# Kernel optimization log

Measured on AMD Instinct MI355X. Metric: run time of the kernel, lower is better.

Reference implementation:

```python
import math
import jax, jax.numpy as jnp
import numpy as np

B, T, D, H, HD, FF = 2, 2048, 768, 12, 64, 3072


def setup_inputs() -> dict:
    key = jax.random.key(0)
    ks = jax.random.split(key, 9)
    s = 0.02  # init scale
    x = jax.random.normal(ks[0], (B, T, D), jnp.float32)
    wq = jax.random.normal(ks[1], (D, D), jnp.float32) * s
    wk = jax.random.normal(ks[2], (D, D), jnp.float32) * s
    wv = jax.random.normal(ks[3], (D, D), jnp.float32) * s
    wo = jax.random.normal(ks[4], (D, D), jnp.float32) * s
    w1 = jax.random.normal(ks[5], (FF, D), jnp.float32) * s
    w2 = jax.random.normal(ks[6], (FF, D), jnp.float32) * s
    w3 = jax.random.normal(ks[7], (D, FF), jnp.float32) * s
    attn_norm_w = jnp.ones((D,), jnp.float32)
    ffn_norm_w = jnp.ones((D,), jnp.float32)
    # interleaved RoPE cache: values pair-repeated along head_dim
    inv_freq = 1.0 / (10000.0 ** (np.arange(0, HD, 2, dtype=np.float32) / HD))
    freqs = np.arange(T, dtype=np.float32)[:, None] * inv_freq[None, :]  # [T, HD/2]
    emb = np.repeat(freqs, 2, axis=-1)  # [T, HD]
    cos = jnp.asarray(np.cos(emb), jnp.float32)[None, None]  # [1,1,T,HD]
    sin = jnp.asarray(np.sin(emb), jnp.float32)[None, None]
    return {"x": x, "wq": wq, "wk": wk, "wv": wv, "wo": wo,
            "w1": w1, "w2": w2, "w3": w3,
            "attn_norm_w": attn_norm_w, "ffn_norm_w": ffn_norm_w,
            "cos": cos, "sin": sin}


def _rmsnorm(x, w, eps=1e-6):
    n = jnp.linalg.norm(x, axis=-1, keepdims=True)
    return w * x / (n / math.sqrt(x.shape[-1]) + eps)


def _rotate_half(x):
    x1, x2 = x[..., ::2], x[..., 1::2]
    return jnp.stack((-x2, x1), axis=-1).reshape(x.shape)


def _attention(x, wq, wk, wv, wo, cos, sin):
    b, t, c = x.shape
    q = (x @ wq.T).reshape(b, t, H, HD).transpose(0, 2, 1, 3)  # [B,H,T,hd]
    k = (x @ wk.T).reshape(b, t, H, HD).transpose(0, 2, 1, 3)
    v = (x @ wv.T).reshape(b, t, H, HD).transpose(0, 2, 1, 3)
    c_, s_ = cos[:, :, :t, :], sin[:, :, :t, :]
    q = q * c_ + _rotate_half(q) * s_
    k = k * c_ + _rotate_half(k) * s_
    att = jnp.einsum('bhqd,bhkd->bhqk', q, k) / math.sqrt(HD)
    mask = jnp.triu(jnp.full((t, t), -jnp.inf, att.dtype), k=1)
    att = jax.nn.softmax(att + mask, axis=-1)
    y = jnp.einsum('bhqk,bhkd->bhqd', att, v)
    y = y.transpose(0, 2, 1, 3).reshape(b, t, c)
    return y @ wo.T


def reference(x, wq, wk, wv, wo, w1, w2, w3, attn_norm_w, ffn_norm_w, cos, sin):
    x = x + _attention(_rmsnorm(x, attn_norm_w), wq, wk, wv, wo, cos, sin)
    h = _rmsnorm(x, ffn_norm_w)
    ff = (jax.nn.silu(h @ w1.T) * (h @ w2.T)) @ w3.T
    return x + ff
```

## Files before the change

### kernel.cpp

```cpp
#include <hip/hip_runtime.h>
#include <hip/hip_bf16.h>
#include <math.h>

typedef __bf16 bf16;
typedef __bf16 bf16x4 __attribute__((ext_vector_type(4)));
typedef __bf16 bf16x8 __attribute__((ext_vector_type(8)));
typedef float floatx4 __attribute__((ext_vector_type(4)));

#define T_ 2048
#define D_ 768
#define H_ 12
#define HD_ 64
#define FF_ 3072
#define LOG2E 1.44269504f
#define LDP 72

__device__ __forceinline__ floatx4 mfma_bf16(bf16x8 a, bf16x8 b, floatx4 c) {
  return __builtin_amdgcn_mfma_f32_16x16x32_bf16(a, b, c, 0, 0, 0);
}

__global__ __launch_bounds__(256)
void cvt_k(const float* __restrict__ wq, const float* __restrict__ wk,
           const float* __restrict__ wv, const float* __restrict__ wo,
           const float* __restrict__ w1, const float* __restrict__ w2,
           const float* __restrict__ w3, bf16* __restrict__ o) {
  const long i = ((long)blockIdx.x * 256 + threadIdx.x) * 8;
  const float* s;
  if      (i <  589824) s = wq + i;
  else if (i < 1179648) s = wk + (i -  589824);
  else if (i < 1769472) s = wv + (i - 1179648);
  else if (i < 2359296) s = wo + (i - 1769472);
  else if (i < 4718592) s = w1 + (i - 2359296);
  else if (i < 7077888) s = w2 + (i - 4718592);
  else                  s = w3 + (i - 7077888);
  const floatx4 a = *(const floatx4*)s;
  const floatx4 b = *(const floatx4*)(s + 4);
  bf16x8 r;
#pragma unroll
  for (int j = 0; j < 4; j++) { r[j] = (bf16)a[j]; r[4 + j] = (bf16)b[j]; }
  *(bf16x8*)&o[i] = r;
}

template<int EP>
__device__ __forceinline__ void gemm128_core(
    const bf16* __restrict__ A, const bf16* __restrict__ W,
    void* __restrict__ C, const float* __restrict__ resid,
    int N, int K, int m0, int n0)
{
  __shared__ __align__(16) bf16 As[128 * LDP];
  __shared__ __align__(16) bf16 Ws[128 * LDP];

  const int tid = threadIdx.x;
  const int lane = tid & 63;
  const int wm = tid >> 7;
  const int wn = (tid >> 6) & 1;
  const int fr = lane & 15;
  const int fk = (lane >> 4) * 8;

  floatx4 acc[4][4] = {};

  const int ar = tid >> 3;
  const int ac = (tid & 7) * 8;
  const bf16* Aptr = A + (long)(m0 + ar) * K + ac;
  const bf16* Wptr = W + (long)(n0 + ar) * K + ac;
  const long rstep = (long)32 * K;

  bf16x8 apf[4], wpf[4];
#pragma unroll
  for (int c = 0; c < 4; c++) apf[c] = *(const bf16x8*)(Aptr + c * rstep);
#pragma unroll
  for (int c = 0; c < 4; c++) wpf[c] = *(const bf16x8*)(Wptr + c * rstep);

  const int ns = K >> 6;
  for (int ks = 0; ks < ns; ks++) {
    __syncthreads();
#pragma unroll
    for (int c = 0; c < 4; c++) *(bf16x8*)&As[(ar + c * 32) * LDP + ac] = apf[c];
#pragma unroll
    for (int c = 0; c < 4; c++) *(bf16x8*)&Ws[(ar + c * 32) * LDP + ac] = wpf[c];
    __syncthreads();
    const long koff = (long)((ks + 1 < ns) ? ks + 1 : ks) * 64;
#pragma unroll
    for (int c = 0; c < 4; c++) apf[c] = *(const bf16x8*)(Aptr + koff + c * rstep);
#pragma unroll
    for (int c = 0; c < 4; c++) wpf[c] = *(const bf16x8*)(Wptr + koff + c * rstep);
#pragma unroll
    for (int kc = 0; kc < 2; kc++) {
      bf16x8 af[4], bfv[4];
#pragma unroll
      for (int i = 0; i < 4; i++) af[i]  = *(const bf16x8*)&As[(wm * 64 + i * 16 + fr) * LDP + kc * 32 + fk];
#pragma unroll
      for (int j = 0; j < 4; j++) bfv[j] = *(const bf16x8*)&Ws[(wn * 64 + j * 16 + fr) * LDP + kc * 32 + fk];
#pragma unroll
      for (int i = 0; i < 4; i++)
#pragma unroll
        for (int j = 0; j < 4; j++)
          acc[i][j] = mfma_bf16(af[i], bfv[j], acc[i][j]);
    }
  }

  const int rb = (lane >> 4) * 4;
#pragma unroll
  for (int i = 0; i < 4; i++) {
#pragma unroll
    for (int j = 0; j < 4; j++) {
      const int n = n0 + wn * 64 + j * 16 + fr;
#pragma unroll
      for (int r = 0; r < 4; r++) {
        const int m = m0 + wm * 64 + i * 16 + rb + r;
        const long idx = (long)m * N + n;
        const float v = acc[i][j][r];
        if (EP == 0) ((bf16*)C)[idx]  = (bf16)v;
        else         ((float*)C)[idx] = v + resid[idx];
      }
    }
  }
}

template<int EP>
__global__ __launch_bounds__(256)
void gemm_bt(const bf16* __restrict__ A, const bf16* __restrict__ W,
             void* __restrict__ C, const float* __restrict__ resid, int N, int K) {
  gemm128_core<EP>(A, W, C, resid, N, K, blockIdx.y * 128, blockIdx.x * 128);
}

__global__ __launch_bounds__(256)
void gemm_qkv(const bf16* __restrict__ h, const bf16* __restrict__ wq,
              const bf16* __restrict__ wk, const bf16* __restrict__ wv,
              bf16* __restrict__ q, bf16* __restrict__ k, bf16* __restrict__ v) {
  const int widx = blockIdx.x / 6;
  const int nb   = blockIdx.x % 6;
  const bf16* W = (widx == 0) ? wq : (widx == 1) ? wk : wv;
  bf16*       O = (widx == 0) ? q  : (widx == 1) ? k  : v;
  gemm128_core<0>(h, W, (void*)O, nullptr, D_, D_, blockIdx.y * 128, nb * 128);
}

template<int EP>
__global__ __launch_bounds__(256)
void gemm_n64(const bf16* __restrict__ A, const bf16* __restrict__ W,
              void* __restrict__ C, const float* __restrict__ resid,
              int N, int K) {
  __shared__ __align__(16) bf16 As[128 * LDP];
  __shared__ __align__(16) bf16 Ws[64 * LDP];

  const int L  = blockIdx.x;
  const int j  = L >> 3;
  const int mb = (L & 7) * 4 + (j / 12);
  const int nb = j % 12;
  const int m0 = mb * 128, n0 = nb * 64;

  const int tid = threadIdx.x;
  const int lane = tid & 63;
  const int wm = tid >> 7;
  const int wn = (tid >> 6) & 1;
  const int fr = lane & 15;
  const int fk = (lane >> 4) * 8;

  floatx4 acc[4][2] = {};

  const int ar = tid >> 3;
  const int ac = (tid & 7) * 8;
  const bf16* Aptr = A + (long)(m0 + ar) * K + ac;
  const bf16* Wptr = W + (long)(n0 + ar) * K + ac;
  const long rstep = (long)32 * K;

  bf16x8 apf[4], wpf[2];
#pragma unroll
  for (int c = 0; c < 4; c++) apf[c] = *(const bf16x8*)(Aptr + c * rstep);
#pragma unroll
  for (int c = 0; c < 2; c++) wpf[c] = *(const bf16x8*)(Wptr + c * rstep);

  const int ns = K >> 6;
  for (int ks = 0; ks < ns; ks++) {
    __syncthreads();
#pragma unroll
    for (int c = 0; c < 4; c++) *(bf16x8*)&As[(ar + c * 32) * LDP + ac] = apf[c];
#pragma unroll
    for (int c = 0; c < 2; c++) *(bf16x8*)&Ws[(ar + c * 32) * LDP + ac] = wpf[c];
    __syncthreads();
    const long koff = (long)((ks + 1 < ns) ? ks + 1 : ks) * 64;
#pragma unroll
    for (int c = 0; c < 4; c++) apf[c] = *(const bf16x8*)(Aptr + koff + c * rstep);
#pragma unroll
    for (int c = 0; c < 2; c++) wpf[c] = *(const bf16x8*)(Wptr + koff + c * rstep);
#pragma unroll
    for (int kc = 0; kc < 2; kc++) {
      bf16x8 af[4], bfv[2];
#pragma unroll
      for (int i = 0; i < 4; i++) af[i]  = *(const bf16x8*)&As[(wm * 64 + i * 16 + fr) * LDP + kc * 32 + fk];
#pragma unroll
      for (int j2 = 0; j2 < 2; j2++) bfv[j2] = *(const bf16x8*)&Ws[(wn * 32 + j2 * 16 + fr) * LDP + kc * 32 + fk];
#pragma unroll
      for (int i = 0; i < 4; i++)
#pragma unroll
        for (int j2 = 0; j2 < 2; j2++)
          acc[i][j2] = mfma_bf16(af[i], bfv[j2], acc[i][j2]);
    }
  }

  const int rb = (lane >> 4) * 4;
#pragma unroll
  for (int i = 0; i < 4; i++) {
#pragma unroll
    for (int j2 = 0; j2 < 2; j2++) {
      const int n = n0 + wn * 32 + j2 * 16 + fr;
#pragma unroll
      for (int r = 0; r < 4; r++) {
        const int m = m0 + wm * 64 + i * 16 + rb + r;
        const long idx = (long)m * N + n;
        const float v = acc[i][j2][r];
        if (EP == 0) ((bf16*)C)[idx]  = (bf16)v;
        else         ((float*)C)[idx] = v + resid[idx];
      }
    }
  }
}

__global__ __launch_bounds__(256)
void rmsnorm_k(const float* __restrict__ x, const float* __restrict__ wt,
               bf16* __restrict__ o) {
  const int row = blockIdx.x;
  const int tid = threadIdx.x;
  const long off = (long)row * D_;
  float vals[3];
  float ss = 0.f;
#pragma unroll
  for (int i = 0; i < 3; i++) {
    vals[i] = x[off + tid + i * 256];
    ss += vals[i] * vals[i];
  }
#pragma unroll
  for (int d = 1; d < 64; d <<= 1) ss += __shfl_xor(ss, d);
  __shared__ float wsum[4];
  if ((tid & 63) == 0) wsum[tid >> 6] = ss;
  __syncthreads();
  const float tot = wsum[0] + wsum[1] + wsum[2] + wsum[3];
  const float inv = 1.0f / (sqrtf(tot * (1.0f / 768.0f)) + 1e-6f);
#pragma unroll
  for (int i = 0; i < 3; i++)
    o[off + tid + i * 256] = (bf16)(vals[i] * inv * wt[tid + i * 256]);
}

__global__ __launch_bounds__(256)
void rope_k(bf16* __restrict__ q, bf16* __restrict__ k,
            const float* __restrict__ cosb, const float* __restrict__ sinb) {
  const int idx = blockIdx.x * 256 + threadIdx.x;
  const int tkn = idx / 384;
  const int p   = idx % 384;
  const int hh  = p >> 5;
  const int i   = p & 31;
  const int pos = tkn & (T_ - 1);
  const long off = (long)tkn * D_ + hh * HD_ + 2 * i;
  const float c0 = cosb[pos * HD_ + 2 * i];
  const float c1 = cosb[pos * HD_ + 2 * i + 1];
  const float s0 = sinb[pos * HD_ + 2 * i];
  const float s1 = sinb[pos * HD_ + 2 * i + 1];
  const float qe = (float)q[off], qo = (float)q[off + 1];
  q[off]     = (bf16)(qe * c0 - qo * s0);
  q[off + 1] = (bf16)(qo * c1 + qe * s1);
  const float ke = (float)k[off], ko = (float)k[off + 1];
  k[off]     = (bf16)(ke * c0 - ko * s0);
  k[off + 1] = (bf16)(ko * c1 + ke * s1);
}

__global__ __launch_bounds__(256)
void vtrans_k(const bf16* __restrict__ v, bf16* __restrict__ vt) {
  const int bh = blockIdx.x >> 5;
  const int tt = blockIdx.x & 31;
  const int b = bh / H_, h = bh % H_;
  __shared__ __align__(16) bf16 Vs[64][72];
  const int tid = threadIdx.x;
  const int row = tid >> 2;
  const int c0  = (tid & 3) * 16;
  const long gin = ((long)(b * T_ + tt * 64 + row)) * D_ + h * HD_ + c0;
  *(bf16x8*)&Vs[row][c0]     = *(const bf16x8*)&v[gin];
  *(bf16x8*)&Vs[row][c0 + 8] = *(const bf16x8*)&v[gin + 8];
  __syncthreads();
  const int hd = tid >> 2;
  const int t0 = (tid & 3) * 16;
  bf16x8 o0, o1;
#pragma unroll
  for (int j = 0; j < 8; j++) { o0[j] = Vs[t0 + j][hd]; o1[j] = Vs[t0 + 8 + j][hd]; }
  const long gout = ((long)(bh * HD_ + hd)) * T_ + tt * 64 + t0;
  *(bf16x8*)&vt[gout]     = o0;
  *(bf16x8*)&vt[gout + 8] = o1;
}

__global__ __launch_bounds__(256, 4)
void flash_attn(const bf16* __restrict__ q, const bf16* __restrict__ k,
                const bf16* __restrict__ vtg, bf16* __restrict__ y) {
  const int bh = blockIdx.x >> 5;
  const int qt = blockIdx.x & 31;
  const int b  = bh / H_;
  const int h  = bh % H_;
  const int q0 = qt * 64;

  __shared__ __align__(16) bf16 Qs[64][72];
  __shared__ __align__(16) bf16 Ks[64][72];
  __shared__ __align__(16) bf16 Vt[64][72];
  __shared__ __align__(16) bf16 Ps[4][16][72];

  const int tid = threadIdx.x, lane = tid & 63, w = tid >> 6;
  const int fr = lane & 15, quad = lane >> 4, fk = quad * 8;
  const long base = ((long)b * T_) * D_ + h * HD_;
  const long vbase = (long)bh * HD_ * T_;

  {
    const int srow = tid >> 2, scol = (tid & 3) * 16;
    const long g = base + (long)(q0 + srow) * D_ + scol;
    *(bf16x8*)&Qs[srow][scol]     = *(const bf16x8*)&q[g];
    *(bf16x8*)&Qs[srow][scol + 8] = *(const bf16x8*)&q[g + 8];
  }

  float m_st = -1e30f, l_st = 0.f;
  floatx4 o[4] = {};
  const float SC = 0.125f * LOG2E;

  for (int t = 0; t <= qt; t++) {
    const int k0 = t * 64;
    __syncthreads();
    {
      const int srow = tid >> 2, scol = (tid & 3) * 16;
      const long kg = base + (long)(k0 + srow) * D_ + scol;
      *(bf16x8*)&Ks[srow][scol]     = *(const bf16x8*)&k[kg];
      *(bf16x8*)&Ks[srow][scol + 8] = *(const bf16x8*)&k[kg + 8];
      const long vg = vbase + (long)srow * T_ + k0 + scol;
      *(bf16x8*)&Vt[srow][scol]     = *(const bf16x8*)&vtg[vg];
      *(bf16x8*)&Vt[srow][scol + 8] = *(const bf16x8*)&vtg[vg + 8];
    }
    __syncthreads();

    floatx4 s[4] = {};
#pragma unroll
    for (int kd = 0; kd < 2; kd++) {
      const bf16x8 bq = *(const bf16x8*)&Qs[w * 16 + fr][kd * 32 + fk];
#pragma unroll
      for (int kt = 0; kt < 4; kt++) {
        const bf16x8 ak = *(const bf16x8*)&Ks[kt * 16 + fr][kd * 32 + fk];
        s[kt] = mfma_bf16(ak, bq, s[kt]);
      }
    }

    if (t == qt) {
      const int qloc = w * 16 + fr;
#pragma unroll
      for (int kt = 0; kt < 4; kt++)
#pragma unroll
        for (int r = 0; r < 4; r++) {
          const int kvloc = kt * 16 + quad * 4 + r;
          s[kt][r] = (kvloc > qloc) ? -1e30f : s[kt][r] * SC;
        }
    } else {
#pragma unroll
      for (int kt = 0; kt < 4; kt++)
#pragma unroll
        for (int r = 0; r < 4; r++) s[kt][r] *= SC;
    }

    float mx = -1e30f;
#pragma unroll
    for (int kt = 0; kt < 4; kt++)
#pragma unroll
      for (int r = 0; r < 4; r++) mx = fmaxf(mx, s[kt][r]);
    mx = fmaxf(mx, __shfl_xor(mx, 16));
    mx = fmaxf(mx, __shfl_xor(mx, 32));
    const float mnew  = fmaxf(m_st, mx);
    const float alpha = exp2f(m_st - mnew);
    m_st = mnew;
    float rs = 0.f;
#pragma unroll
    for (int kt = 0; kt < 4; kt++)
#pragma unroll
      for (int r = 0; r < 4; r++) {
        const float pv = exp2f(s[kt][r] - mnew);
        s[kt][r] = pv;
        rs += pv;
      }
    rs += __shfl_xor(rs, 16);
    rs += __shfl_xor(rs, 32);
    l_st = l_st * alpha + rs;
#pragma unroll
    for (int ht = 0; ht < 4; ht++) o[ht] *= alpha;

#pragma unroll
    for (int kt = 0; kt < 4; kt++) {
      bf16x4 pk;
#pragma unroll
      for (int r = 0; r < 4; r++) pk[r] = (bf16)s[kt][r];
      *(bf16x4*)&Ps[w][fr][kt * 16 + quad * 4] = pk;
    }

#pragma unroll
    for (int kq = 0; kq < 2; kq++) {
      const bf16x8 bp = *(const bf16x8*)&Ps[w][fr][kq * 32 + fk];
#pragma unroll
      for (int ht = 0; ht < 4; ht++) {
        const bf16x8 av = *(const bf16x8*)&Vt[ht * 16 + fr][kq * 32 + fk];
        o[ht] = mfma_bf16(av, bp, o[ht]);
      }
    }
  }

  const float inv = 1.0f / l_st;
  const long yrow = base + (long)(q0 + w * 16 + fr) * D_;
#pragma unroll
  for (int ht = 0; ht < 4; ht++) {
    bf16x4 pk;
#pragma unroll
    for (int r = 0; r < 4; r++) pk[r] = (bf16)(o[ht][r] * inv);
    *(bf16x4*)&y[yrow + ht * 16 + quad * 4] = pk;
  }
}

__global__ __launch_bounds__(256)
void silu_mul_k(bf16* __restrict__ g1, const bf16* __restrict__ g2) {
  const long i0 = ((long)blockIdx.x * 256 + threadIdx.x) * 8;
  bf16x8 a = *(bf16x8*)&g1[i0];
  bf16x8 b = *(const bf16x8*)&g2[i0];
#pragma unroll
  for (int j = 0; j < 8; j++) {
    const float x = (float)a[j];
    const float s = x / (1.f + exp2f(-x * LOG2E));
    a[j] = (bf16)(s * (float)b[j]);
  }
  *(bf16x8*)&g1[i0] = a;
}

extern "C" void kernel_launch(void* const* d_in, const int* in_sizes, int n_in,
                              void* d_out, int out_size, void* d_ws, size_t ws_size,
                              hipStream_t stream) {
  const float* x    = (const float*)d_in[0];
  const float* wq   = (const float*)d_in[1];
  const float* wk   = (const float*)d_in[2];
  const float* wv   = (const float*)d_in[3];
  const float* wo   = (const float*)d_in[4];
  const float* w1   = (const float*)d_in[5];
  const float* w2   = (const float*)d_in[6];
  const float* w3   = (const float*)d_in[7];
  const float* anw  = (const float*)d_in[8];
  const float* fnw  = (const float*)d_in[9];
  const float* cosb = (const float*)d_in[10];
  const float* sinb = (const float*)d_in[11];

  char* ws = (char*)d_ws;
  bf16*  wb  = (bf16*)(ws + 0);
  bf16*  wqb = wb;
  bf16*  wkb = wb +  589824;
  bf16*  wvb = wb + 1179648;
  bf16*  wob = wb + 1769472;
  bf16*  w1b = wb + 2359296;
  bf16*  w2b = wb + 4718592;
  bf16*  w3b = wb + 7077888;
  bf16*  qb  = (bf16*)(ws + 18874368);
  bf16*  kb  = (bf16*)(ws + 25165824);
  bf16*  vb  = (bf16*)(ws + 31457280);
  bf16*  yb  = (bf16*)(ws + 37748736);
  bf16*  hn  = (bf16*)(ws + 44040192);
  float* xm  = (float*)(ws + 50331648);
  bf16*  g1  = (bf16*)(ws + 62914560);
  bf16*  vt  = (bf16*)(ws + 62914560);
  bf16*  g2  = qb;

  cvt_k<<<4608, 256, 0, stream>>>(wq, wk, wv, wo, w1, w2, w3, wb);
  rmsnorm_k<<<4096, 256, 0, stream>>>(x, anw, hn);
  gemm_qkv<<<dim3(18, 32), 256, 0, stream>>>(hn, wqb, wkb, wvb, qb, kb, vb);
  rope_k<<<6144, 256, 0, stream>>>(qb, kb, cosb, sinb);
  vtrans_k<<<768, 256, 0, stream>>>(vb, vt);
  flash_attn<<<768, 256, 0, stream>>>(qb, kb, vt, yb);
  gemm_n64<1><<<384, 256, 0, stream>>>(yb, wob, (void*)xm, x, 768, 768);
  rmsnorm_k<<<4096, 256, 0, stream>>>(xm, fnw, hn);
  gemm_bt<0><<<dim3(24, 32), 256, 0, stream>>>(hn, w1b, (void*)g1, nullptr, 3072, 768);
  gemm_bt<0><<<dim3(24, 32), 256, 0, stream>>>(hn, w2b, (void*)g2, nullptr, 3072, 768);
  silu_mul_k<<<6144, 256, 0, stream>>>(g1, g2);
  gemm_n64<1><<<384, 256, 0, stream>>>(g1, w3b, d_out, xm, 768, 3072);
}
```

Measured before the change: 347.5 us.

## Split causal attention over KV chunks and fuse W1/W2 GEMMs with SiLU

Flash attention is split into up to four KV chunks per query tile (1920 blocks) to balance the causal triangle, with a new combine kernel merging the partial outputs using the max and sum statistics. The two FFN up-projections are computed in one kernel sharing the A tile, with the SiLU-multiply applied in the epilogue, removing separate g1/g2 buffers and the elementwise kernel. The cost is extra float32 partial-output traffic for attention and higher register use in the fused GEMM.

```diff
diff --git a/kernel.cpp b/kernel.cpp
--- a/kernel.cpp
+++ b/kernel.cpp
@@ -41,11 +41,9 @@
   *(bf16x8*)&o[i] = r;
 }
 
-template<int EP>
 __device__ __forceinline__ void gemm128_core(
     const bf16* __restrict__ A, const bf16* __restrict__ W,
-    void* __restrict__ C, const float* __restrict__ resid,
-    int N, int K, int m0, int n0)
+    bf16* __restrict__ C, int N, int K, int m0, int n0)
 {
   __shared__ __align__(16) bf16 As[128 * LDP];
   __shared__ __align__(16) bf16 Ws[128 * LDP];
@@ -101,27 +99,16 @@
 
   const int rb = (lane >> 4) * 4;
 #pragma unroll
-  for (int i = 0; i < 4; i++) {
+  for (int i = 0; i < 4; i++)
 #pragma unroll
     for (int j = 0; j < 4; j++) {
       const int n = n0 + wn * 64 + j * 16 + fr;
 #pragma unroll
       for (int r = 0; r < 4; r++) {
         const int m = m0 + wm * 64 + i * 16 + rb + r;
-        const long idx = (long)m * N + n;
-        const float v = acc[i][j][r];
-        if (EP == 0) ((bf16*)C)[idx]  = (bf16)v;
-        else         ((float*)C)[idx] = v + resid[idx];
+        C[(long)m * N + n] = (bf16)acc[i][j][r];
       }
     }
-  }
-}
-
-template<int EP>
-__global__ __launch_bounds__(256)
-void gemm_bt(const bf16* __restrict__ A, const bf16* __restrict__ W,
-             void* __restrict__ C, const float* __restrict__ resid, int N, int K) {
-  gemm128_core<EP>(A, W, C, resid, N, K, blockIdx.y * 128, blockIdx.x * 128);
 }
 
 __global__ __launch_bounds__(256)
@@ -132,13 +119,12 @@
   const int nb   = blockIdx.x % 6;
   const bf16* W = (widx == 0) ? wq : (widx == 1) ? wk : wv;
   bf16*       O = (widx == 0) ? q  : (widx == 1) ? k  : v;
-  gemm128_core<0>(h, W, (void*)O, nullptr, D_, D_, blockIdx.y * 128, nb * 128);
-}
-
-template<int EP>
+  gemm128_core(h, W, O, D_, D_, blockIdx.y * 128, nb * 128);
+}
+
 __global__ __launch_bounds__(256)
 void gemm_n64(const bf16* __restrict__ A, const bf16* __restrict__ W,
-              void* __restrict__ C, const float* __restrict__ resid,
+              float* __restrict__ C, const float* __restrict__ resid,
               int N, int K) {
   __shared__ __align__(16) bf16 As[128 * LDP];
   __shared__ __align__(16) bf16 Ws[64 * LDP];
@@ -200,7 +186,7 @@
 
   const int rb = (lane >> 4) * 4;
 #pragma unroll
-  for (int i = 0; i < 4; i++) {
+  for (int i = 0; i < 4; i++)
 #pragma unroll
     for (int j2 = 0; j2 < 2; j2++) {
       const int n = n0 + wn * 32 + j2 * 16 + fr;
@@ -208,12 +194,96 @@
       for (int r = 0; r < 4; r++) {
         const int m = m0 + wm * 64 + i * 16 + rb + r;
         const long idx = (long)m * N + n;
-        const float v = acc[i][j2][r];
-        if (EP == 0) ((bf16*)C)[idx]  = (bf16)v;
-        else         ((float*)C)[idx] = v + resid[idx];
+        C[idx] = acc[i][j2][r] + resid[idx];
       }
     }
-  }
+}
+
+__global__ __launch_bounds__(256)
+void gemm_w12(const bf16* __restrict__ A, const bf16* __restrict__ W1,
+              const bf16* __restrict__ W2, bf16* __restrict__ G) {
+  __shared__ __align__(16) bf16 As[128 * LDP];
+  __shared__ __align__(16) bf16 W1s[64 * LDP];
+  __shared__ __align__(16) bf16 W2s[64 * LDP];
+
+  const int L  = blockIdx.x;
+  const int j  = L >> 3;
+  const int nb = (L & 7) * 6 + (j >> 5);
+  const int mb = j & 31;
+  const int m0 = mb * 128, n0 = nb * 64;
+  const int K = D_;
+
+  const int tid = threadIdx.x;
+  const int lane = tid & 63;
+  const int wm = tid >> 7;
+  const int wn = (tid >> 6) & 1;
+  const int fr = lane & 15;
+  const int fk = (lane >> 4) * 8;
+
+  floatx4 acc1[4][2] = {}, acc2[4][2] = {};
+
+  const int ar = tid >> 3;
+  const int ac = (tid & 7) * 8;
+  const bf16* Aptr  = A  + (long)(m0 + ar) * K + ac;
+  const bf16* W1ptr = W1 + (long)(n0 + ar) * K + ac;
+  const bf16* W2ptr = W2 + (long)(n0 + ar) * K + ac;
+  const long rstep = (long)32 * K;
+
+  bf16x8 apf[4], w1pf[2], w2pf[2];
+#pragma unroll
+  for (int c = 0; c < 4; c++) apf[c] = *(const bf16x8*)(Aptr + c * rstep);
+#pragma unroll
+  for (int c = 0; c < 2; c++) { w1pf[c] = *(const bf16x8*)(W1ptr + c * rstep);
+                                w2pf[c] = *(const bf16x8*)(W2ptr + c * rstep); }
+
+  const int ns = K >> 6;
+  for (int ks = 0; ks < ns; ks++) {
+    __syncthreads();
+#pragma unroll
+    for (int c = 0; c < 4; c++) *(bf16x8*)&As[(ar + c * 32) * LDP + ac] = apf[c];
+#pragma unroll
+    for (int c = 0; c < 2; c++) { *(bf16x8*)&W1s[(ar + c * 32) * LDP + ac] = w1pf[c];
+                                  *(bf16x8*)&W2s[(ar + c * 32) * LDP + ac] = w2pf[c]; }
+    __syncthreads();
+    const long koff = (long)((ks + 1 < ns) ? ks + 1 : ks) * 64;
+#pragma unroll
+    for (int c = 0; c < 4; c++) apf[c] = *(const bf16x8*)(Aptr + koff + c * rstep);
+#pragma unroll
+    for (int c = 0; c < 2; c++) { w1pf[c] = *(const bf16x8*)(W1ptr + koff + c * rstep);
+                                  w2pf[c] = *(const bf16x8*)(W2ptr + koff + c * rstep); }
+#pragma unroll
+    for (int kc = 0; kc < 2; kc++) {
+      bf16x8 af[4], b1[2], b2[2];
+#pragma unroll
+      for (int i = 0; i < 4; i++) af[i] = *(const bf16x8*)&As[(wm * 64 + i * 16 + fr) * LDP + kc * 32 + fk];
+#pragma unroll
+      for (int j2 = 0; j2 < 2; j2++) { b1[j2] = *(const bf16x8*)&W1s[(wn * 32 + j2 * 16 + fr) * LDP + kc * 32 + fk];
+                                       b2[j2] = *(const bf16x8*)&W2s[(wn * 32 + j2 * 16 + fr) * LDP + kc * 32 + fk]; }
+#pragma unroll
+      for (int i = 0; i < 4; i++)
+#pragma unroll
+        for (int j2 = 0; j2 < 2; j2++) {
+          acc1[i][j2] = mfma_bf16(af[i], b1[j2], acc1[i][j2]);
+          acc2[i][j2] = mfma_bf16(af[i], b2[j2], acc2[i][j2]);
+        }
+    }
+  }
+
+  const int rb = (lane >> 4) * 4;
+#pragma unroll
+  for (int i = 0; i < 4; i++)
+#pragma unroll
+    for (int j2 = 0; j2 < 2; j2++) {
+      const int n = n0 + wn * 32 + j2 * 16 + fr;
+#pragma unroll
+      for (int r = 0; r < 4; r++) {
+        const int m = m0 + wm * 64 + i * 16 + rb + r;
+        const float a1 = acc1[i][j2][r];
+        const float a2 = acc2[i][j2][r];
+        const float s = a1 / (1.f + exp2f(-a1 * LOG2E));
+        G[(long)m * FF_ + n] = (bf16)(s * a2);
+      }
+    }
 }
 
 __global__ __launch_bounds__(256)
@@ -288,12 +358,21 @@
 
 __global__ __launch_bounds__(256, 4)
 void flash_attn(const bf16* __restrict__ q, const bf16* __restrict__ k,
-                const bf16* __restrict__ vtg, bf16* __restrict__ y) {
-  const int bh = blockIdx.x >> 5;
-  const int qt = blockIdx.x & 31;
+                const bf16* __restrict__ vtg, float* __restrict__ po,
+                float* __restrict__ pm, float* __restrict__ pl) {
+  const int gid = blockIdx.x;
+  const int bh = gid / 80;
+  const int r  = gid % 80;
+  int qt, c;
+  if (r < 8)       { qt = r; c = 0; }
+  else if (r < 24) { qt = 8 + ((r - 8) >> 1); c = (r - 8) & 1; }
+  else if (r < 48) { const int u = r - 24; const int d = u / 3; qt = 16 + d; c = u - d * 3; }
+  else             { const int u = r - 48; qt = 24 + (u >> 2); c = u & 3; }
   const int b  = bh / H_;
   const int h  = bh % H_;
   const int q0 = qt * 64;
+  const int tbeg = c * 8;
+  const int tend = (tbeg + 7 < qt) ? tbeg + 7 : qt;
 
   __shared__ __align__(16) bf16 Qs[64][72];
   __shared__ __align__(16) bf16 Ks[64][72];
@@ -316,7 +395,7 @@
   floatx4 o[4] = {};
   const float SC = 0.125f * LOG2E;
 
-  for (int t = 0; t <= qt; t++) {
+  for (int t = tbeg; t <= tend; t++) {
     const int k0 = t * 64;
     __syncthreads();
     {
@@ -346,22 +425,22 @@
 #pragma unroll
       for (int kt = 0; kt < 4; kt++)
 #pragma unroll
-        for (int r = 0; r < 4; r++) {
-          const int kvloc = kt * 16 + quad * 4 + r;
-          s[kt][r] = (kvloc > qloc) ? -1e30f : s[kt][r] * SC;
+        for (int r2 = 0; r2 < 4; r2++) {
+          const int kvloc = kt * 16 + quad * 4 + r2;
+          s[kt][r2] = (kvloc > qloc) ? -1e30f : s[kt][r2] * SC;
         }
     } else {
 #pragma unroll
       for (int kt = 0; kt < 4; kt++)
 #pragma unroll
-        for (int r = 0; r < 4; r++) s[kt][r] *= SC;
+        for (int r2 = 0; r2 < 4; r2++) s[kt][r2] *= SC;
     }
 
     float mx = -1e30f;
 #pragma unroll
     for (int kt = 0; kt < 4; kt++)
 #pragma unroll
-      for (int r = 0; r < 4; r++) mx = fmaxf(mx, s[kt][r]);
+      for (int r2 = 0; r2 < 4; r2++) mx = fmaxf(mx, s[kt][r2]);
     mx = fmaxf(mx, __shfl_xor(mx, 16));
     mx = fmaxf(mx, __shfl_xor(mx, 32));
     const float mnew  = fmaxf(m_st, mx);
@@ -371,9 +450,9 @@
 #pragma unroll
     for (int kt = 0; kt < 4; kt++)
 #pragma unroll
-      for (int r = 0; r < 4; r++) {
-        const float pv = exp2f(s[kt][r] - mnew);
-        s[kt][r] = pv;
+      for (int r2 = 0; r2 < 4; r2++) {
+        const float pv = exp2f(s[kt][r2] - mnew);
+        s[kt][r2] = pv;
         rs += pv;
       }
     rs += __shfl_xor(rs, 16);
@@ -386,7 +465,7 @@
     for (int kt = 0; kt < 4; kt++) {
       bf16x4 pk;
 #pragma unroll
-      for (int r = 0; r < 4; r++) pk[r] = (bf16)s[kt][r];
+      for (int r2 = 0; r2 < 4; r2++) pk[r2] = (bf16)s[kt][r2];
       *(bf16x4*)&Ps[w][fr][kt * 16 + quad * 4] = pk;
     }
 
@@ -401,29 +480,58 @@
     }
   }
 
-  const float inv = 1.0f / l_st;
-  const long yrow = base + (long)(q0 + w * 16 + fr) * D_;
-#pragma unroll
-  for (int ht = 0; ht < 4; ht++) {
-    bf16x4 pk;
-#pragma unroll
-    for (int r = 0; r < 4; r++) pk[r] = (bf16)(o[ht][r] * inv);
-    *(bf16x4*)&y[yrow + ht * 16 + quad * 4] = pk;
-  }
-}
-
-__global__ __launch_bounds__(256)
-void silu_mul_k(bf16* __restrict__ g1, const bf16* __restrict__ g2) {
-  const long i0 = ((long)blockIdx.x * 256 + threadIdx.x) * 8;
-  bf16x8 a = *(bf16x8*)&g1[i0];
-  bf16x8 b = *(const bf16x8*)&g2[i0];
-#pragma unroll
-  for (int j = 0; j < 8; j++) {
-    const float x = (float)a[j];
-    const float s = x / (1.f + exp2f(-x * LOG2E));
-    a[j] = (bf16)(s * (float)b[j]);
-  }
-  *(bf16x8*)&g1[i0] = a;
+  const int qq = w * 16 + fr;
+  const long pg = (long)gid * 4096 + qq * 64;
+#pragma unroll
+  for (int ht = 0; ht < 4; ht++)
+    *(floatx4*)&po[pg + ht * 16 + quad * 4] = o[ht];
+  if (quad == 0) { pm[gid * 64 + qq] = m_st; pl[gid * 64 + qq] = l_st; }
+}
+
+__global__ __launch_bounds__(256)
+void flash_comb(const float* __restrict__ po, const float* __restrict__ pm,
+                const float* __restrict__ pl, bf16* __restrict__ y) {
+  const int bh = blockIdx.x >> 5;
+  const int qt = blockIdx.x & 31;
+  const int b = bh / H_, h = bh % H_;
+  const int nc = (qt >> 3) + 1;
+  int bse;
+  if      (qt <  8) bse = qt;
+  else if (qt < 16) bse = 8  + 2 * (qt - 8);
+  else if (qt < 24) bse = 24 + 3 * (qt - 16);
+  else              bse = 48 + 4 * (qt - 24);
+  const int g0 = bh * 80 + bse;
+
+  const int t = threadIdx.x;
+  const int qq = t >> 2, hg = (t & 3) * 16;
+
+  float M = -1e30f;
+  for (int c2 = 0; c2 < nc; c2++) M = fmaxf(M, pm[(g0 + c2) * 64 + qq]);
+  float l = 0.f;
+  floatx4 o[4] = {};
+  for (int c2 = 0; c2 < nc; c2++) {
+    const float wgt = exp2f(pm[(g0 + c2) * 64 + qq] - M);
+    l += wgt * pl[(g0 + c2) * 64 + qq];
+    const long pg = (long)(g0 + c2) * 4096 + qq * 64 + hg;
+#pragma unroll
+    for (int j = 0; j < 4; j++) {
+      const floatx4 t4 = *(const floatx4*)&po[pg + j * 4];
+#pragma unroll
+      for (int e = 0; e < 4; e++) o[j][e] += wgt * t4[e];
+    }
+  }
+  const float inv = 1.f / l;
+  bf16x8 r0, r1;
+#pragma unroll
+  for (int e = 0; e < 4; e++) {
+    r0[e]     = (bf16)(o[0][e] * inv);
+    r0[4 + e] = (bf16)(o[1][e] * inv);
+    r1[e]     = (bf16)(o[2][e] * inv);
+    r1[4 + e] = (bf16)(o[3][e] * inv);
+  }
+  const long yoff = ((long)b * T_ + qt * 64 + qq) * D_ + h * HD_ + hg;
+  *(bf16x8*)&y[yoff]     = r0;
+  *(bf16x8*)&y[yoff + 8] = r1;
 }
 
 extern "C" void kernel_launch(void* const* d_in, const int* in_sizes, int n_in,
@@ -453,24 +561,25 @@
   bf16*  w3b = wb + 7077888;
   bf16*  qb  = (bf16*)(ws + 18874368);
   bf16*  kb  = (bf16*)(ws + 25165824);
-  bf16*  vb  = (bf16*)(ws + 31457280);
+  bf16*  vt  = (bf16*)(ws + 31457280);
   bf16*  yb  = (bf16*)(ws + 37748736);
   bf16*  hn  = (bf16*)(ws + 44040192);
   float* xm  = (float*)(ws + 50331648);
-  bf16*  g1  = (bf16*)(ws + 62914560);
-  bf16*  vt  = (bf16*)(ws + 62914560);
-  bf16*  g2  = qb;
+  bf16*  g   = (bf16*)(ws + 62914560);
+  bf16*  vb  = (bf16*)(ws + 62914560);
+  float* po  = (float*)(ws + 50331648);
+  float* pm  = (float*)(ws + 81788928);
+  float* pl  = (float*)(ws + 82280448);
 
   cvt_k<<<4608, 256, 0, stream>>>(wq, wk, wv, wo, w1, w2, w3, wb);
   rmsnorm_k<<<4096, 256, 0, stream>>>(x, anw, hn);
   gemm_qkv<<<dim3(18, 32), 256, 0, stream>>>(hn, wqb, wkb, wvb, qb, kb, vb);
   rope_k<<<6144, 256, 0, stream>>>(qb, kb, cosb, sinb);
   vtrans_k<<<768, 256, 0, stream>>>(vb, vt);
-  flash_attn<<<768, 256, 0, stream>>>(qb, kb, vt, yb);
-  gemm_n64<1><<<384, 256, 0, stream>>>(yb, wob, (void*)xm, x, 768, 768);
+  flash_attn<<<1920, 256, 0, stream>>>(qb, kb, vt, po, pm, pl);
+  flash_comb<<<768, 256, 0, stream>>>(po, pm, pl, yb);
+  gemm_n64<<<384, 256, 0, stream>>>(yb, wob, xm, x, 768, 768);
   rmsnorm_k<<<4096, 256, 0, stream>>>(xm, fnw, hn);
-  gemm_bt<0><<<dim3(24, 32), 256, 0, stream>>>(hn, w1b, (void*)g1, nullptr, 3072, 768);
-  gemm_bt<0><<<dim3(24, 32), 256, 0, stream>>>(hn, w2b, (void*)g2, nullptr, 3072, 768);
-  silu_mul_k<<<6144, 256, 0, stream>>>(g1, g2);
-  gemm_n64<1><<<384, 256, 0, stream>>>(g1, w3b, d_out, xm, 768, 3072);
-}
+  gemm_w12<<<1536, 256, 0, stream>>>(hn, w1b, w2b, g);
+  gemm_n64<<<384, 256, 0, stream>>>(g, w3b, (float*)d_out, xm, 768, 3072);
+}
```

Measured after the change: 322.0 us. 7.3% less time.
